# Kernel tuning notes

Measured on AMD Instinct MI355X. Metric: run time of the kernel, lower is better.

## Reference

```python
import jax, jax.numpy as jnp
import numpy as np

# ---- Cayley-Dickson octonion multiplication tables (SIGN_TABLE, WEIGHT_IDX) ----
def _cd_conj(a):
    n = a.shape[0]
    if n == 1:
        return a
    h = n // 2
    return np.concatenate([_cd_conj(a[:h]), -a[h:]])

def _cd_mul(a, b):
    n = a.shape[0]
    if n == 1:
        return a * b
    h = n // 2
    a1, a2 = a[:h], a[h:]
    c1, c2 = b[:h], b[h:]
    # (a1,a2)(c1,c2) = (a1 c1 - conj(c2) a2, c2 a1 + a2 conj(c1))
    return np.concatenate([_cd_mul(a1, c1) - _cd_mul(_cd_conj(c2), a2),
                           _cd_mul(c2, a1) + _cd_mul(a2, _cd_conj(c1))])

def _octonion_tables():
    signs = np.zeros((8, 8), dtype=np.float32)
    widx = np.zeros((8, 8), dtype=np.int32)
    for i in range(8):
        for j in range(8):
            ei = np.zeros(8); ei[i] = 1.0
            ej = np.zeros(8); ej[j] = 1.0
            p = _cd_mul(ei, ej)
            k = int(np.argmax(np.abs(p)))  # == i ^ j
            signs[i, j] = np.sign(p[k])
            widx[i, j] = k
    return jnp.asarray(signs), jnp.asarray(widx)

SIGNS, WIDX = _octonion_tables()


def ternary_ste(W):
    # BitNet-style per-matrix ternary quantization with straight-through estimator.
    s = jnp.mean(jnp.abs(W), axis=(-2, -1), keepdims=True) + 1e-8
    Wq = jnp.clip(jnp.round(W / s), -1.0, 1.0) * s
    return W + jax.lax.stop_gradient(Wq - W)


def oct_linear(x, W):
    # x: [B,T,C] split into 8 parts of C/8; out_i = sum_j sign[i,j] * x_j @ Wq[i^j]
    B, T, C = x.shape
    c8 = C // 8
    x8 = x.reshape(B, T, 8, c8)
    Wq = ternary_ste(W)          # [8, c8, c8]
    Wg = Wq[WIDX]                # [8, 8, c8, c8]
    out = jnp.einsum('ij,btjc,ijcd->btid', SIGNS, x8, Wg)
    return out.reshape(B, T, C)


def apply_rope(q, freqs_cos, freqs_sin):
    # q: [B,T,H,D]; complex pairs are (q[...,2k], q[...,2k+1])
    qe, qo = q[..., 0::2], q[..., 1::2]
    cos = freqs_cos[None, :, None, :]
    sin = freqs_sin[None, :, None, :]
    oe = qe * cos - qo * sin
    oo = qe * sin + qo * cos
    return jnp.stack([oe, oo], axis=-1).reshape(q.shape)


def setup_inputs() -> dict:
    key = jax.random.key(0)
    ks = jax.random.split(key, 8)
    B, T, C, H = 4, 1024, 2048, 16
    D = C // H           # 128
    c8 = C // 8          # 256
    x = jax.random.normal(ks[0], (B, T, C), dtype=jnp.float32)
    # RoPE tables (theta = 10000)
    inv = 1.0 / (10000.0 ** (jnp.arange(0, D, 2, dtype=jnp.float32) / D))
    ang = jnp.arange(T, dtype=jnp.float32)[:, None] * inv[None, :]   # [T, D/2]
    freqs_cos = jnp.cos(ang)
    freqs_sin = jnp.sin(ang)
    wq = jax.random.normal(ks[1], (8, c8, c8), dtype=jnp.float32) * 0.02
    wk = jax.random.normal(ks[2], (8, c8, c8), dtype=jnp.float32) * 0.02
    wv = jax.random.normal(ks[3], (8, c8, c8), dtype=jnp.float32) * 0.02
    wo = jax.random.normal(ks[4], (8, c8, c8), dtype=jnp.float32) * 0.02
    mixer_W = jax.random.normal(ks[5], (8, D, D), dtype=jnp.float32) * 0.02
    mixer_beta = jnp.ones((D,), dtype=jnp.float32) * 0.1
    return {"x": x, "freqs_cos": freqs_cos, "freqs_sin": freqs_sin,
            "wq": wq, "wk": wk, "wv": wv, "wo": wo,
            "mixer_W": mixer_W, "mixer_beta": mixer_beta}


def reference(x, freqs_cos, freqs_sin, wq, wk, wv, wo, mixer_W, mixer_beta):
    B, T, C = x.shape
    H = 16
    D = C // H
    q = oct_linear(x, wq).reshape(B, T, H, D)
    k = oct_linear(x, wk).reshape(B, T, H, D)
    v = oct_linear(x, wv).reshape(B, T, H, D)
    q = apply_rope(q, freqs_cos, freqs_sin)
    k = apply_rope(k, freqs_cos, freqs_sin)
    q, k, v = (jnp.transpose(t, (0, 2, 1, 3)) for t in (q, k, v))  # [B,H,T,D]
    # causal SDPA
    scale = 1.0 / jnp.sqrt(jnp.asarray(D, dtype=q.dtype))
    scores = jnp.einsum('bhqd,bhkd->bhqk', q, k) * scale
    mask = jnp.tril(jnp.ones((T, T), dtype=bool))
    scores = jnp.where(mask, scores, jnp.asarray(-1e30, dtype=scores.dtype))
    probs = jax.nn.softmax(scores, axis=-1)
    y = jnp.einsum('bhqk,bhkd->bhqd', probs, v)  # [B,H,T,D]
    # octonion head mixing per group of 8 heads
    G = H // 8
    y8 = y.reshape(B, G, 8, T, D)
    Wg = mixer_W[WIDX]  # [8,8,D,D]
    y8 = jnp.einsum('ij,bgjtd,ijde->bgite', SIGNS, y8, Wg) * mixer_beta
    y = y8.reshape(B, H, T, D)
    y = jnp.transpose(y, (0, 2, 1, 3)).reshape(B, T, C)
    return oct_linear(y, wo)
```

## Files before the change

### kernel.cpp

```cpp
#include <hip/hip_runtime.h>
#include <math.h>

#define CDIM 2048
#define QKVW 6144

typedef __bf16 bf16x8 __attribute__((ext_vector_type(8)));
typedef __bf16 bf16x4 __attribute__((ext_vector_type(4)));
typedef float  f32x4  __attribute__((ext_vector_type(4)));
typedef float  f32x16 __attribute__((ext_vector_type(16)));

__device__ __constant__ float SIGNS_c[64] = {
  1,  1,  1,  1,  1,  1,  1,  1,
  1, -1,  1, -1,  1, -1, -1,  1,
  1, -1, -1,  1,  1,  1, -1, -1,
  1,  1, -1, -1,  1, -1,  1, -1,
  1, -1, -1, -1, -1,  1,  1,  1,
  1,  1, -1,  1, -1, -1, -1,  1,
  1,  1,  1, -1, -1,  1, -1, -1,
  1, -1,  1,  1, -1, -1,  1, -1
};

__device__ __forceinline__ void load_lds16(const void* g, void* lp) {
  __builtin_amdgcn_global_load_lds(
      (const __attribute__((address_space(1))) unsigned int*)g,
      (__attribute__((address_space(3))) unsigned int*)lp, 16, 0, 0);
}

__device__ __forceinline__ void wg_barrier() {
  asm volatile("" ::: "memory");
  __builtin_amdgcn_s_barrier();
  asm volatile("" ::: "memory");
}

__device__ __forceinline__ unsigned pack2(float a, float b) {
  union { __bf16 h[2]; unsigned u; } x;
  x.h[0] = (__bf16)a; x.h[1] = (__bf16)b; return x.u;
}

__global__ __launch_bounds__(256)
void scale_part(const float* __restrict__ wq, const float* __restrict__ wk,
                const float* __restrict__ wv, const float* __restrict__ wo,
                double* __restrict__ part) {
  int bid = blockIdx.x;
  int which = bid >> 6, m = (bid >> 3) & 7, seg = bid & 7;
  const float* W = (which == 0) ? wq : (which == 1) ? wk : (which == 2) ? wv : wo;
  const float4* w4 = (const float4*)(W + (m << 16) + seg * 8192);
  double acc = 0.0;
  #pragma unroll
  for (int i = 0; i < 8; ++i) {
    float4 v = w4[threadIdx.x + i * 256];
    acc += (double)fabsf(v.x) + (double)fabsf(v.y) +
           (double)fabsf(v.z) + (double)fabsf(v.w);
  }
  __shared__ double red[256];
  red[threadIdx.x] = acc;
  __syncthreads();
  for (int s = 128; s > 0; s >>= 1) {
    if (threadIdx.x < s) red[threadIdx.x] += red[threadIdx.x + s];
    __syncthreads();
  }
  if (threadIdx.x == 0) part[bid] = red[0];
}

__global__ void scale_fin(const double* __restrict__ part, double* __restrict__ s8) {
  int t = threadIdx.x;
  if (t < 32) {
    double a = 0.0;
    #pragma unroll
    for (int i = 0; i < 8; ++i) a += part[t * 8 + i];
    s8[t] = a / 65536.0 + 1e-8;
  }
}

__global__ void build_oct3(const float* __restrict__ wq, const float* __restrict__ wk,
                           const float* __restrict__ wv, const double* __restrict__ s8,
                           __bf16* __restrict__ MT) {
  int z = blockIdx.y;
  const float* W = (z == 0) ? wq : (z == 1) ? wk : wv;
  const double* sp = s8 + z * 8;
  __bf16* out = MT + (size_t)z * 4194304;
  int idx = blockIdx.x * 256 + threadIdx.x;
  int row = idx & 2047, col = idx >> 11;
  int i = col >> 8, d = col & 255, j = row >> 8, c = row & 255;
  int m = i ^ j;
  double s = sp[m];
  double q = rint((double)W[(m << 16) + (c << 8) + d] / s);
  q = fmin(fmax(q, -1.0), 1.0);
  out[idx] = (__bf16)(SIGNS_c[i * 8 + j] * (float)(q * s));
}

__global__ void build_oct_T(const float* __restrict__ W, const double* __restrict__ s8,
                            __bf16* __restrict__ MT) {
  int idx = blockIdx.x * 256 + threadIdx.x;
  int row = idx & 2047, col = idx >> 11;
  int i = col >> 8, d = col & 255, j = row >> 8, c = row & 255;
  int m = i ^ j;
  double s = s8[m];
  double q = rint((double)W[(m << 16) + (c << 8) + d] / s);
  q = fmin(fmax(q, -1.0), 1.0);
  MT[idx] = (__bf16)(SIGNS_c[i * 8 + j] * (float)(q * s));
}

__global__ void build_mix_plain(const float* __restrict__ Wm, const float* __restrict__ beta,
                                __bf16* __restrict__ M) {
  int idx = blockIdx.x * 256 + threadIdx.x;
  int kl = idx & 1023, kpl = idx >> 10;
  int j = kpl >> 7, dd = kpl & 127;
  int i = kl >> 7, e = kl & 127;
  M[idx] = (__bf16)(SIGNS_c[i * 8 + j] * Wm[((i ^ j) << 14) + (dd << 7) + e] * beta[e]);
}

__global__ void cast_x(const float* __restrict__ x, __bf16* __restrict__ xb) {
  int i = blockIdx.x * 256 + threadIdx.x;
  float4 v = *(const float4*)(x + (size_t)i * 4);
  bf16x4 o;
  o[0] = (__bf16)v.x; o[1] = (__bf16)v.y; o[2] = (__bf16)v.z; o[3] = (__bf16)v.w;
  *(bf16x4*)(xb + (size_t)i * 4) = o;
}

__global__ __launch_bounds__(512, 2)
void gemm_qkv8(const __bf16* __restrict__ A, const __bf16* __restrict__ BT,
               __bf16* __restrict__ C) {
  __shared__ __align__(16) char smem[131072];
  int tid = threadIdx.x;
  int w = tid >> 6, l = tid & 63, hi = l >> 4, lo = l & 15;
  int wm = w >> 2, wn = w & 3;
  int lin = blockIdx.x;
  int xcd = lin & 7, idx = lin >> 3;
  int cy = xcd >> 2, cx = xcd & 3;
  int iby = idx >> 3, ibx = idx & 7;
  int bm = (cy * 8 + iby) * 256;
  int bn = (cx * 8 + ibx) * 192;
  const char* Ab = (const char*)A + (size_t)bm * 4096;
  const char* Bb = (const char*)BT + (size_t)bn * 4096;

  int sw = (((lo & 1) << 2) + hi) ^ (lo >> 1);

  int se_r[2], se_g[2], se_rb[2];
  #pragma unroll
  for (int q = 0; q < 2; ++q) {
    int e = q * 512 + tid;
    int lr = e >> 3, sl = e & 7;
    int x = sl ^ (lr & 7);
    se_r[q] = lr * 2 + (x >> 2);
    se_g[q] = x & 3;
    se_rb[q] = se_r[q] < 192 ? se_r[q] : 191;
  }
  int dstoff[2] = { (0 * 512 + w * 64) * 16, (1 * 512 + w * 64) * 16 };

  f32x4 acc[8][3];
  #pragma unroll
  for (int m = 0; m < 8; ++m)
    #pragma unroll
    for (int n = 0; n < 3; ++n) acc[m][n] = (f32x4){0.f, 0.f, 0.f, 0.f};
  bf16x8 bfr[3];

  #define STG(MAT, TT, KH) do {                                                  \
    char* dst_ = smem + ((TT) & 1) * 65536 + (MAT) * 32768 + (KH) * 16384;       \
    const char* gb_ = (MAT) ? Bb : Ab;                                           \
    _Pragma("unroll")                                                            \
    for (int q = 0; q < 2; ++q) {                                                \
      int r_ = (MAT) ? se_rb[q] : se_r[q];                                       \
      load_lds16(gb_ + (size_t)r_ * 4096 + ((TT) * 64 + (KH) * 32) * 2 + se_g[q] * 16, \
                 dst_ + dstoff[q]);                                              \
    }                                                                            \
  } while (0)

  #define QUAD(TT, KH, MSUB, READB) do {                                         \
    const char* ar_ = smem + ((TT) & 1) * 65536 + (KH) * 16384;                  \
    const char* br_ = ar_ + 32768;                                               \
    if (READB) {                                                                 \
      _Pragma("unroll")                                                          \
      for (int n = 0; n < 3; ++n)                                                \
        bfr[n] = *(const bf16x8*)(br_ + (wn * 24 + n * 8 + (lo >> 1)) * 128 + sw * 16); \
    }                                                                            \
    bf16x8 afr[4];                                                               \
    _Pragma("unroll")                                                            \
    for (int m = 0; m < 4; ++m)                                                  \
      afr[m] = *(const bf16x8*)(ar_ + (wm * 64 + (MSUB) * 32 + m * 8 + (lo >> 1)) * 128 + sw * 16); \
    __builtin_amdgcn_s_setprio(1);                                               \
    _Pragma("unroll")                                                            \
    for (int m = 0; m < 4; ++m)                                                  \
      _Pragma("unroll")                                                          \
      for (int n = 0; n < 3; ++n)                                                \
        acc[(MSUB) * 4 + m][n] =                                                 \
            __builtin_amdgcn_mfma_f32_16x16x32_bf16(afr[m], bfr[n], acc[(MSUB) * 4 + m][n], 0, 0, 0); \
    __builtin_amdgcn_s_setprio(0);                                               \
  } while (0)

  #define LGK0() asm volatile("s_waitcnt lgkmcnt(0)" ::: "memory")
  #define VMW8() asm volatile("s_waitcnt vmcnt(8)" ::: "memory")
  #define VMW4() asm volatile("s_waitcnt vmcnt(4)" ::: "memory")
  #define VMW0() asm volatile("s_waitcnt vmcnt(0)" ::: "memory")

  STG(0, 0, 0); STG(1, 0, 0);
  STG(0, 0, 1); STG(1, 0, 1);
  STG(0, 1, 0); STG(1, 1, 0);
  VMW8();
  wg_barrier();

  #define GITER(T0, LAST) do {                                                   \
     STG(0, (T0) + 1, 1); QUAD((T0), 0, 0, 1); wg_barrier();            \
     STG(1, (T0) + 1, 1); QUAD((T0), 0, 1, 0); LGK0(); VMW8(); wg_barrier(); \
     if (!(LAST)) { STG(0, (T0) + 2, 0); } QUAD((T0), 1, 0, 1); wg_barrier(); \
     if (!(LAST)) { STG(1, (T0) + 2, 0); } QUAD((T0), 1, 1, 0); LGK0(); \
              if (LAST) { VMW4(); } else { VMW8(); } wg_barrier();               \
     if (!(LAST)) { STG(0, (T0) + 2, 1); } QUAD((T0) + 1, 0, 0, 1); wg_barrier(); \
     if (!(LAST)) { STG(1, (T0) + 2, 1); } QUAD((T0) + 1, 0, 1, 0); LGK0(); \
              if (LAST) { VMW0(); } else { VMW8(); } wg_barrier();               \
     if (!(LAST)) { STG(0, (T0) + 3, 0); } QUAD((T0) + 1, 1, 0, 1); wg_barrier(); \
     if (!(LAST)) { STG(1, (T0) + 3, 0); } QUAD((T0) + 1, 1, 1, 0);     \
              if (!(LAST)) { LGK0(); VMW8(); wg_barrier(); }                     \
  } while (0)

  for (int i = 0; i < 15; ++i) GITER(2 * i, false);
  GITER(30, true);

  #undef GITER
  #undef STG
  #undef QUAD
  #undef VMW8
  #undef VMW4

  #pragma unroll
  for (int mm = 0; mm < 8; ++mm)
    #pragma unroll
    for (int n = 0; n < 3; ++n)
      #pragma unroll
      for (int r = 0; r < 4; ++r) {
        int row = bm + wm * 128 + mm * 16 + hi * 4 + r;
        int col = bn + wn * 48 + n * 16 + lo;
        C[(size_t)row * QKVW + col] = (__bf16)acc[mm][n][r];
      }
}

__global__ __launch_bounds__(512, 2)
void gemm_fin8(const __bf16* __restrict__ A, const __bf16* __restrict__ BT,
               float* __restrict__ C) {
  __shared__ __align__(16) char smem[98304];
  int tid = threadIdx.x;
  int w = tid >> 6, l = tid & 63, hi = l >> 4, lo = l & 15;
  int wm = w >> 2, wn = w & 3;
  int lin = blockIdx.x;
  int xcd = lin & 7, idx = lin >> 3;
  int cy = xcd >> 1, cx = xcd & 1;
  int iby = idx >> 2, ibx = idx & 3;
  int bm = (cy * 8 + iby) * 128;
  int bn = (cx * 4 + ibx) * 256;
  const char* Ab = (const char*)A + (size_t)bm * 12288;
  const char* Bb = (const char*)BT + (size_t)bn * 4096;

  int sw = (((lo & 1) << 2) + hi) ^ (lo >> 1);

  int se_r[2], se_g[2];
  #pragma unroll
  for (int q = 0; q < 2; ++q) {
    int e = q * 512 + tid;
    int lr = e >> 3, sl = e & 7;
    int x = sl ^ (lr & 7);
    se_r[q] = lr * 2 + (x >> 2);
    se_g[q] = x & 3;
  }
  int dstoff[2] = { (0 * 512 + w * 64) * 16, (1 * 512 + w * 64) * 16 };

  f32x4 acc[4][4];
  #pragma unroll
  for (int m = 0; m < 4; ++m)
    #pragma unroll
    for (int n = 0; n < 4; ++n) acc[m][n] = (f32x4){0.f, 0.f, 0.f, 0.f};
  bf16x8 bfr[4];

  #define STG(MAT, TT, KH) do {                                                  \
    char* ab_ = smem + ((TT) & 1) * 49152;                                       \
    char* dst_ = (MAT) ? (ab_ + 16384 + (KH) * 16384) : (ab_ + (KH) * 8192);     \
    const char* gb_ = (MAT) ? Bb : Ab;                                           \
    size_t ld_ = (MAT) ? 4096 : 12288;                                           \
    int nq_ = (MAT) ? 2 : 1;                                                     \
    _Pragma("unroll")                                                            \
    for (int q = 0; q < 2; ++q)                                                  \
      if (q < nq_)                                                               \
        load_lds16(gb_ + (size_t)se_r[q] * ld_ + ((TT) * 64 + (KH) * 32) * 2 + se_g[q] * 16, \
                   dst_ + dstoff[q]);                                            \
  } while (0)

  #define QUAD(TT, KH, MSUB, READB) do {                                         \
    const char* ab_ = smem + ((TT) & 1) * 49152;                                 \
    const char* ar_ = ab_ + (KH) * 8192;                                         \
    const char* br_ = ab_ + 16384 + (KH) * 16384;                                \
    if (READB) {                                                                 \
      _Pragma("unroll")                                                          \
      for (int n = 0; n < 4; ++n)                                                \
        bfr[n] = *(const bf16x8*)(br_ + (wn * 32 + n * 8 + (lo >> 1)) * 128 + sw * 16); \
    }                                                                            \
    bf16x8 afr[2];                                                               \
    _Pragma("unroll")                                                            \
    for (int m = 0; m < 2; ++m)                                                  \
      afr[m] = *(const bf16x8*)(ar_ + (wm * 32 + (MSUB) * 16 + m * 8 + (lo >> 1)) * 128 + sw * 16); \
    __builtin_amdgcn_s_setprio(1);                                               \
    _Pragma("unroll")                                                            \
    for (int m = 0; m < 2; ++m)                                                  \
      _Pragma("unroll")                                                          \
      for (int n = 0; n < 4; ++n)                                                \
        acc[(MSUB) * 2 + m][n] =                                                 \
            __builtin_amdgcn_mfma_f32_16x16x32_bf16(afr[m], bfr[n], acc[(MSUB) * 2 + m][n], 0, 0, 0); \
    __builtin_amdgcn_s_setprio(0);                                               \
  } while (0)

  #define VMW6() asm volatile("s_waitcnt vmcnt(6)" ::: "memory")
  #define VMW3() asm volatile("s_waitcnt vmcnt(3)" ::: "memory")

  STG(0, 0, 0); STG(1, 0, 0);
  STG(0, 0, 1); STG(1, 0, 1);
  STG(0, 1, 0); STG(1, 1, 0);
  VMW6();
  wg_barrier();

  #define GITER(T0, LAST) do {                                                   \
     STG(0, (T0) + 1, 1); QUAD((T0), 0, 0, 1); wg_barrier();            \
     STG(1, (T0) + 1, 1); QUAD((T0), 0, 1, 0); LGK0(); VMW6(); wg_barrier(); \
     if (!(LAST)) { STG(0, (T0) + 2, 0); } QUAD((T0), 1, 0, 1); wg_barrier(); \
     if (!(LAST)) { STG(1, (T0) + 2, 0); } QUAD((T0), 1, 1, 0); LGK0(); \
              if (LAST) { VMW3(); } else { VMW6(); } wg_barrier();               \
     if (!(LAST)) { STG(0, (T0) + 2, 1); } QUAD((T0) + 1, 0, 0, 1); wg_barrier(); \
     if (!(LAST)) { STG(1, (T0) + 2, 1); } QUAD((T0) + 1, 0, 1, 0); LGK0(); \
              if (LAST) { VMW0(); } else { VMW6(); } wg_barrier();               \
     if (!(LAST)) { STG(0, (T0) + 3, 0); } QUAD((T0) + 1, 1, 0, 1); wg_barrier(); \
     if (!(LAST)) { STG(1, (T0) + 3, 0); } QUAD((T0) + 1, 1, 1, 0);     \
              if (!(LAST)) { LGK0(); VMW6(); wg_barrier(); }                     \
  } while (0)

  for (int i = 0; i < 15; ++i) GITER(2 * i, false);
  GITER(30, true);

  #undef GITER
  #undef STG
  #undef QUAD
  #undef VMW6
  #undef VMW3
  #undef LGK0
  #undef VMW0

  #pragma unroll
  for (int mm = 0; mm < 4; ++mm)
    #pragma unroll
    for (int n = 0; n < 4; ++n)
      #pragma unroll
      for (int r = 0; r < 4; ++r) {
        int row = bm + wm * 64 + mm * 16 + hi * 4 + r;
        int col = bn + wn * 64 + n * 16 + lo;
        C[(size_t)row * 2048 + col] = acc[mm][n][r];
      }
}

template<int BN, int NBY, int NBX, int CBY, int CBX, int KLEN, int LDA, int OUT_BF16>
__global__ __launch_bounds__(512, 2)
void gemm_ps(const __bf16* __restrict__ A, const __bf16* __restrict__ BT,
             void* __restrict__ Cout, int az, int cz, int ldc) {
  constexpr int FN = BN / 64;
  constexpr int LB = (BN > 128) ? 2 : 1;
  constexpr int VC = 2 + LB;
  constexpr int BUFSZ = 16384 + 8192 * LB;
  constexpr int CGX = NBX / CBX;
  static_assert((NBY / CBY) * CGX == 8, "chunk grid must be 8 XCDs");
  __shared__ __align__(16) char smem[2 * BUFSZ];
  int tid = threadIdx.x;
  int w = tid >> 6, l = tid & 63, hi = l >> 4, lo = l & 15;
  int wm = w >> 2, wn = w & 3;
  int lin = blockIdx.x;
  int xcd = lin & 7, idx = lin >> 3;
  int cy = xcd / CGX, cx = xcd % CGX;
  int iby = idx / CBX, ibx = idx % CBX;
  int bm = (cy * CBY + iby) * 256;
  int bn = (cx * CBX + ibx) * BN;
  const char* Ab = (const char*)(A + (size_t)blockIdx.y * az) + (size_t)bm * LDA * 2;
  const char* Bb = (const char*)BT + (size_t)bn * KLEN * 2;

  int sw = (((lo & 1) << 2) + hi) ^ (lo >> 1);
  int base_a = (wm * 64 + (lo >> 1)) * 128 + sw * 16;
  int base_b = 16384 + (wn * (BN / 8) + (lo >> 1)) * 128 + sw * 16;

  int se_r[2], se_g[2];
  #pragma unroll
  for (int q = 0; q < 2; ++q) {
    int e = q * 512 + tid;
    int lr = e >> 3, sl = e & 7;
    int x = sl ^ (lr & 7);
    se_r[q] = lr * 2 + (x >> 2);
    se_g[q] = x & 3;
  }
  int dstoff[2] = { (0 * 512 + w * 64) * 16, (1 * 512 + w * 64) * 16 };

  f32x4 acc[8][FN];
  #pragma unroll
  for (int m = 0; m < 8; ++m)
    #pragma unroll
    for (int n = 0; n < FN; ++n) acc[m][n] = (f32x4){0.f, 0.f, 0.f, 0.f};

  #define STAGE(BUFI, K0) do {                                                   \
    char* As_ = smem + (BUFI) * BUFSZ;                                           \
    char* Bs_ = As_ + 16384;                                                     \
    _Pragma("unroll")                                                            \
    for (int q = 0; q < 2; ++q)                                                  \
      load_lds16(Ab + (size_t)se_r[q] * (LDA * 2) + (size_t)(K0) * 2 + se_g[q] * 16, \
                 As_ + dstoff[q]);                                               \
    _Pragma("unroll")                                                            \
    for (int q = 0; q < LB; ++q)                                                 \
      load_lds16(Bb + (size_t)se_r[q] * (KLEN * 2) + (size_t)(K0) * 2 + se_g[q] * 16, \
                 Bs_ + dstoff[q]);                                               \
  } while (0)

  #define WAITVC() do {                                                \
    if constexpr (VC == 4) asm volatile("s_waitcnt vmcnt(4)" ::: "memory"); \
    else                   asm volatile("s_waitcnt vmcnt(3)" ::: "memory"); \
  } while (0)

  constexpr int NT = KLEN / 32;
  STAGE(0, 0);
  STAGE(1, 32);
  WAITVC();
  wg_barrier();

  for (int t = 0; t < NT; ++t) {
    char* buf = smem + (t & 1) * BUFSZ;
    bf16x8 bfr[FN], afr[8];
    #pragma unroll
    for (int n = 0; n < FN; ++n) bfr[n] = *(const bf16x8*)(buf + base_b + n * 1024);
    #pragma unroll
    for (int m = 0; m < 8; ++m) afr[m] = *(const bf16x8*)(buf + base_a + m * 1024);
    __builtin_amdgcn_s_setprio(1);
    #pragma unroll
    for (int m = 0; m < 4; ++m)
      #pragma unroll
      for (int n = 0; n < FN; ++n)
        acc[m][n] = __builtin_amdgcn_mfma_f32_16x16x32_bf16(afr[m], bfr[n], acc[m][n], 0, 0, 0);
    __builtin_amdgcn_s_setprio(0);
    asm volatile("s_waitcnt lgkmcnt(0)" ::: "memory");
    wg_barrier();

    if (t + 2 < NT) STAGE(t & 1, (t + 2) * 32);
    __builtin_amdgcn_s_setprio(1);
    #pragma unroll
    for (int m = 4; m < 8; ++m)
      #pragma unroll
      for (int n = 0; n < FN; ++n)
        acc[m][n] = __builtin_amdgcn_mfma_f32_16x16x32_bf16(afr[m], bfr[n], acc[m][n], 0, 0, 0);
    __builtin_amdgcn_s_setprio(0);
    if (t + 2 < NT) { WAITVC(); }
    else            { asm volatile("s_waitcnt vmcnt(0)" ::: "memory"); }
    wg_barrier();
  }
  #undef STAGE
  #undef WAITVC

  #pragma unroll
  for (int m = 0; m < 8; ++m)
    #pragma unroll
    for (int n = 0; n < FN; ++n)
      #pragma unroll
      for (int r = 0; r < 4; ++r) {
        int row = bm + wm * 64 + m * 16 + hi * 4 + r;
        int col = bn + wn * (BN / 4) + n * 16 + lo;
        if (OUT_BF16)
          ((__bf16*)Cout)[(size_t)blockIdx.y * cz + (size_t)(bm + wm * 128 + m * 16 + hi * 4 + r) * ldc + col] = (__bf16)acc[m][n][r];
        else
          ((float*)Cout)[(size_t)blockIdx.y * cz + (size_t)(bm + wm * 128 + m * 16 + hi * 4 + r) * ldc + col] = acc[m][n][r];
      }
}

__global__ void rope_bf16(__bf16* __restrict__ QKV,
                          const float* __restrict__ fc, const float* __restrict__ fs) {
  int idx = blockIdx.x * 256 + threadIdx.x;
  int pg = idx & 15;
  int h = (idx >> 4) & 15;
  int n = idx >> 8;
  int t = n & 1023;
  float4 c4 = *(const float4*)(fc + t * 64 + pg * 4);
  float4 s4 = *(const float4*)(fs + t * 64 + pg * 4);
  float c[4] = {c4.x, c4.y, c4.z, c4.w};
  float s[4] = {s4.x, s4.y, s4.z, s4.w};
  size_t ofs = (size_t)n * QKVW + h * 128 + pg * 8;
  bf16x8 q = *(bf16x8*)(QKV + ofs);
  bf16x8 k = *(bf16x8*)(QKV + 2048 + ofs);
  bf16x8 oq, ok;
  #pragma unroll
  for (int j = 0; j < 4; ++j) {
    float x = (float)q[2 * j], y = (float)q[2 * j + 1];
    oq[2 * j]     = (__bf16)(x * c[j] - y * s[j]);
    oq[2 * j + 1] = (__bf16)(x * s[j] + y * c[j]);
    float u = (float)k[2 * j], vv = (float)k[2 * j + 1];
    ok[2 * j]     = (__bf16)(u * c[j] - vv * s[j]);
    ok[2 * j + 1] = (__bf16)(u * s[j] + vv * c[j]);
  }
  *(bf16x8*)(QKV + ofs) = oq;
  *(bf16x8*)(QKV + 2048 + ofs) = ok;
}

__global__ __launch_bounds__(256)
void transpose_v(const __bf16* __restrict__ QKV, __bf16* __restrict__ VT) {
  __shared__ __bf16 tile[64][136];
  int tid = threadIdx.x;
  int tt = blockIdx.x;
  int bh = blockIdx.y;
  int b = bh >> 4, h = bh & 15;
  int t0 = tt * 64;
  #pragma unroll
  for (int q = 0; q < 4; ++q) {
    int i = q * 256 + tid;
    int tr = i >> 4, u = i & 15;
    bf16x8 v = *(const bf16x8*)(QKV + (size_t)(b * 1024 + t0 + tr) * QKVW + 4096 + h * 128 + u * 8);
    *(bf16x8*)&tile[tr][u * 8] = v;
  }
  __syncthreads();
  #pragma unroll
  for (int q = 0; q < 4; ++q) {
    int i = q * 256 + tid;
    int d = i >> 3, tu = i & 7;
    bf16x8 o;
    #pragma unroll
    for (int jj = 0; jj < 8; ++jj) o[jj] = tile[tu * 8 + jj][d];
    *(bf16x8*)(VT + ((size_t)bh * 128 + d) * 1024 + t0 + tu * 8) = o;
  }
}

__global__ __launch_bounds__(256, 2)
void attn_mfma2(__bf16* __restrict__ QKV, const __bf16* __restrict__ VT) {
  __shared__ __align__(16) char smem[65536];
  int tid = threadIdx.x;
  int w = tid >> 6, l = tid & 63;
  int lo = l & 31, hv = l >> 5;
  int wgid = blockIdx.x;
  int xcd = wgid & 7, idx = wgid >> 3;
  int s = idx & 7, j = s >> 1, odd = s & 1, hi5 = idx >> 5;
  int base = hi5 ? 7 - j : j;
  int qt = odd ? 7 - base : base;
  int bh = xcd * 8 + (idx >> 3);
  int b = bh >> 4, h = bh & 15;
  int qb = qt * 128;
  int wq0 = qb + w * 32;
  int qrow = wq0 + lo;
  const __bf16* qp = QKV + (size_t)(b * 1024 + qrow) * QKVW + h * 128;
  bf16x8 qf[8];
  #pragma unroll
  for (int c = 0; c < 8; ++c) qf[c] = *(const bf16x8*)(qp + c * 16 + hv * 8);

  f32x16 o[4];
  #pragma unroll
  for (int n = 0; n < 4; ++n)
    #pragma unroll
    for (int r = 0; r < 16; ++r) o[n][r] = 0.f;
  float mrun = -1e30f, lrun = 0.f;
  const float SCL = 0.08838834764831845f * 1.4426950408889634f;
  int src0 = lo, src1 = 32 + lo;
  int nt = 2 * qt + 2;

  #define ASTAGE(BUF, KT) do {                                                   \
    _Pragma("unroll")                                                            \
    for (int i = 0; i < 4; ++i) {                                                \
      int e = i * 256 + tid;                                                     \
      int row = e >> 4, g = e & 15;                                              \
      int gs = g ^ (row & 7);                                                    \
      const char* src = (const char*)QKV +                                       \
          ((size_t)(b * 1024 + (KT) * 64 + row) * QKVW + 2048 + h * 128) * 2 + gs * 16; \
      load_lds16(src, smem + (BUF) * 16384 + (i * 256 + w * 64) * 16);           \
    }                                                                            \
    _Pragma("unroll")                                                            \
    for (int i = 0; i < 4; ++i) {                                                \
      int e = i * 256 + tid;                                                     \
      int row = e >> 3, g = e & 7;                                               \
      int gs = g ^ (row & 7);                                                    \
      const char* src = (const char*)VT +                                        \
          ((size_t)(bh * 128 + row) * 1024 + (KT) * 64) * 2 + gs * 16;           \
      load_lds16(src, smem + 32768 + (BUF) * 16384 + (i * 256 + w * 64) * 16);   \
    }                                                                            \
  } while (0)

  ASTAGE(0, 0);
  asm volatile("s_waitcnt vmcnt(0)" ::: "memory");
  wg_barrier();

  for (int kt = 0; kt < nt; ++kt) {
    int cur = kt & 1;
    if (kt + 1 < nt) ASTAGE(cur ^ 1, kt + 1);
    int k0 = kt * 64;
    char* Ks  = smem + cur * 16384;
    char* VTs = smem + 32768 + cur * 16384;

    if (k0 <= wq0 + 31) {
      f32x16 sT[2];
      #pragma unroll
      for (int kk = 0; kk < 2; ++kk) {
        #pragma unroll
        for (int r = 0; r < 16; ++r) sT[kk][r] = 0.f;
        #pragma unroll
        for (int c = 0; c < 8; ++c) {
          bf16x8 kf = *(const bf16x8*)(Ks + (kk * 32 + lo) * 256 + (((2 * c + hv) ^ (lo & 7)) * 16));
          sT[kk] = __builtin_amdgcn_mfma_f32_32x32x16_bf16(kf, qf[c], sT[kk], 0, 0, 0);
        }
      }
      bool diag = (k0 + 63 > wq0);
      float pv[2][16];
      #pragma unroll
      for (int kk = 0; kk < 2; ++kk)
        #pragma unroll
        for (int r = 0; r < 16; ++r) {
          float v = sT[kk][r] * SCL;
          if (diag) {
            int kg = k0 + kk * 32 + (r & 3) + 8 * (r >> 2) + 4 * hv;
            if (kg > qrow) v = -1e30f;
          }
          pv[kk][r] = v;
        }
      float mx = pv[0][0];
      #pragma unroll
      for (int kk = 0; kk < 2; ++kk)
        #pragma unroll
        for (int r = 0; r < 16; ++r) mx = fmaxf(mx, pv[kk][r]);
      mx = fmaxf(mx, __shfl_xor(mx, 32, 64));
      if (!__all(mx <= mrun + 8.f)) {
        float mnew = fmaxf(mrun, mx);
        float fac = exp2f(mrun - mnew);
        lrun *= fac;
        #pragma unroll
        for (int n = 0; n < 4; ++n)
          #pragma unroll
          for (int r = 0; r < 16; ++r) o[n][r] *= fac;
        mrun = mnew;
      }
      float rs = 0.f;
      #pragma unroll
      for (int kk = 0; kk < 2; ++kk)
        #pragma unroll
        for (int r = 0; r < 16; ++r) {
          float p = exp2f(pv[kk][r] - mrun);
          pv[kk][r] = p;
          rs += p;
        }
      rs += __shfl_xor(rs, 32, 64);
      lrun += rs;

      unsigned pk[2][4][2];
      #pragma unroll
      for (int kk = 0; kk < 2; ++kk)
        #pragma unroll
        for (int m = 0; m < 4; ++m)
          #pragma unroll
          for (int u = 0; u < 2; ++u)
            pk[kk][m][u] = pack2(pv[kk][m * 4 + 2 * u], pv[kk][m * 4 + 2 * u + 1]);

      #pragma unroll
      for (int kk = 0; kk < 2; ++kk) {
        #pragma unroll
        for (int s2 = 0; s2 < 2; ++s2) {
          unsigned a0 = __shfl(pk[kk][2 * s2][0], src0, 64);
          unsigned b0 = __shfl(pk[kk][2 * s2 + 1][0], src0, 64);
          unsigned a1 = __shfl(pk[kk][2 * s2][1], src0, 64);
          unsigned b1 = __shfl(pk[kk][2 * s2 + 1][1], src0, 64);
          unsigned a2 = __shfl(pk[kk][2 * s2][0], src1, 64);
          unsigned b2 = __shfl(pk[kk][2 * s2 + 1][0], src1, 64);
          unsigned a3 = __shfl(pk[kk][2 * s2][1], src1, 64);
          unsigned b3 = __shfl(pk[kk][2 * s2 + 1][1], src1, 64);
          union { unsigned u[4]; bf16x8 v; } pb;
          pb.u[0] = hv ? b0 : a0;
          pb.u[1] = hv ? b1 : a1;
          pb.u[2] = hv ? b2 : a2;
          pb.u[3] = hv ? b3 : a3;
          int ks16 = 2 * kk + s2;
          #pragma unroll
          for (int n = 0; n < 4; ++n) {
            bf16x8 vf = *(const bf16x8*)(VTs + (n * 32 + lo) * 128 +
                                         (((2 * ks16 + hv) ^ (lo & 7)) * 16));
            o[n] = __builtin_amdgcn_mfma_f32_32x32x16_bf16(vf, pb.v, o[n], 0, 0, 0);
          }
        }
      }
    }
    asm volatile("s_waitcnt vmcnt(0)" ::: "memory");
    wg_barrier();
  }
  #undef ASTAGE

  float inv = 1.f / lrun;
  __bf16* op = QKV + (size_t)(b * 1024 + qrow) * QKVW + h * 128;
  #pragma unroll
  for (int n = 0; n < 4; ++n)
    #pragma unroll
    for (int m4 = 0; m4 < 4; ++m4) {
      bf16x4 ov;
      #pragma unroll
      for (int jj = 0; jj < 4; ++jj) ov[jj] = (__bf16)(o[n][m4 * 4 + jj] * inv);
      *(bf16x4*)(op + n * 32 + 8 * m4 + 4 * hv) = ov;
    }
}

extern "C" void kernel_launch(void* const* d_in, const int* in_sizes, int n_in,
                              void* d_out, int out_size, void* d_ws, size_t ws_size,
                              hipStream_t stream) {
  const float* x    = (const float*)d_in[0];
  const float* fc   = (const float*)d_in[1];
  const float* fs   = (const float*)d_in[2];
  const float* wq   = (const float*)d_in[3];
  const float* wk   = (const float*)d_in[4];
  const float* wv   = (const float*)d_in[5];
  const float* wo   = (const float*)d_in[6];
  const float* wm   = (const float*)d_in[7];
  const float* beta = (const float*)d_in[8];

  char* wsb = (char*)d_ws;
  __bf16* xb      = (__bf16*)(wsb);
  __bf16* MTqkv   = (__bf16*)(wsb + 16777216L);
  __bf16* QKV     = (__bf16*)(wsb + 41943040L);
  __bf16* VTb     = (__bf16*)(wsb + 92274688L);
  double* s8      = (double*)(wsb + 109051904L);
  double* part    = (double*)(wsb + 109052160L);
  __bf16* MTwo    = (__bf16*)(wsb);
  __bf16* BTfused = (__bf16*)(wsb + 8388608L);
  __bf16* MTmixP  = MTqkv;

  dim3 blk(256);

  cast_x<<<8192, blk, 0, stream>>>(x, xb);
  scale_part<<<256, blk, 0, stream>>>(wq, wk, wv, wo, part);
  scale_fin<<<1, dim3(64), 0, stream>>>(part, s8);
  build_oct3<<<dim3(16384, 3), blk, 0, stream>>>(wq, wk, wv, s8, MTqkv);

  gemm_qkv8<<<512, dim3(512), 0, stream>>>(xb, MTqkv, QKV);

  build_oct_T<<<16384, blk, 0, stream>>>(wo, s8 + 24, MTwo);
  build_mix_plain<<<4096, blk, 0, stream>>>(wm, beta, MTmixP);
  gemm_ps<128, 8, 8, 2, 4, 1024, 2048, 1>
      <<<dim3(64, 2), dim3(512), 0, stream>>>(MTwo, MTmixP, BTfused, 1024, 1024, 2048);

  rope_bf16<<<4096, blk, 0, stream>>>(QKV, fc, fs);
  transpose_v<<<dim3(16, 64), blk, 0, stream>>>(QKV, VTb);

  attn_mfma2<<<dim3(512), blk, 0, stream>>>(QKV, VTb);

  gemm_fin8<<<256, dim3(512), 0, stream>>>(QKV, BTfused, (float*)d_out);
}
```

Before: 305.9 us.

## Fuse RoPE into QKV GEMM epilogue, merge cast with scale reduction

Applies rotary embedding inside the QKV GEMM epilogue, using a lane shuffle to fetch the pair partner, so the standalone rope kernel and its extra read and write of Q/K are gone. The x cast and the weight-scale partial reduction are merged into one launch, and the scale finish kernel also writes reciprocals so the build kernels multiply instead of doing a double divide. The multiply by a reciprocal can round differently from the divide at ternary rounding boundaries. RoPE is now computed in fp32 before the bf16 store, which differs slightly from the old order of storing bf16 first and then rotating.

Result: slower. 321.0 us (+5.0%).

```diff
diff --git a/kernel.cpp b/kernel.cpp
--- a/kernel.cpp
+++ b/kernel.cpp
@@ -38,10 +38,20 @@
 }
 
 __global__ __launch_bounds__(256)
-void scale_part(const float* __restrict__ wq, const float* __restrict__ wk,
+void cast_scale(const float* __restrict__ x, __bf16* __restrict__ xb,
+                const float* __restrict__ wq, const float* __restrict__ wk,
                 const float* __restrict__ wv, const float* __restrict__ wo,
                 double* __restrict__ part) {
-  int bid = blockIdx.x;
+  __shared__ double red[256];
+  if (blockIdx.x < 8192) {
+    int i = blockIdx.x * 256 + threadIdx.x;
+    float4 v = *(const float4*)(x + (size_t)i * 4);
+    bf16x4 o;
+    o[0] = (__bf16)v.x; o[1] = (__bf16)v.y; o[2] = (__bf16)v.z; o[3] = (__bf16)v.w;
+    *(bf16x4*)(xb + (size_t)i * 4) = o;
+    return;
+  }
+  int bid = blockIdx.x - 8192;
   int which = bid >> 6, m = (bid >> 3) & 7, seg = bid & 7;
   const float* W = (which == 0) ? wq : (which == 1) ? wk : (which == 2) ? wv : wo;
   const float4* w4 = (const float4*)(W + (m << 16) + seg * 8192);
@@ -52,7 +62,6 @@
     acc += (double)fabsf(v.x) + (double)fabsf(v.y) +
            (double)fabsf(v.z) + (double)fabsf(v.w);
   }
-  __shared__ double red[256];
   red[threadIdx.x] = acc;
   __syncthreads();
   for (int s = 128; s > 0; s >>= 1) {
@@ -62,43 +71,45 @@
   if (threadIdx.x == 0) part[bid] = red[0];
 }
 
-__global__ void scale_fin(const double* __restrict__ part, double* __restrict__ s8) {
+__global__ void scale_fin(const double* __restrict__ part, double* __restrict__ s8,
+                          double* __restrict__ rs8) {
   int t = threadIdx.x;
   if (t < 32) {
     double a = 0.0;
     #pragma unroll
     for (int i = 0; i < 8; ++i) a += part[t * 8 + i];
-    s8[t] = a / 65536.0 + 1e-8;
+    double s = a / 65536.0 + 1e-8;
+    s8[t] = s;
+    rs8[t] = 1.0 / s;
   }
 }
 
 __global__ void build_oct3(const float* __restrict__ wq, const float* __restrict__ wk,
                            const float* __restrict__ wv, const double* __restrict__ s8,
-                           __bf16* __restrict__ MT) {
+                           const double* __restrict__ rs8, __bf16* __restrict__ MT) {
   int z = blockIdx.y;
   const float* W = (z == 0) ? wq : (z == 1) ? wk : wv;
   const double* sp = s8 + z * 8;
+  const double* rp = rs8 + z * 8;
   __bf16* out = MT + (size_t)z * 4194304;
   int idx = blockIdx.x * 256 + threadIdx.x;
   int row = idx & 2047, col = idx >> 11;
   int i = col >> 8, d = col & 255, j = row >> 8, c = row & 255;
   int m = i ^ j;
-  double s = sp[m];
-  double q = rint((double)W[(m << 16) + (c << 8) + d] / s);
+  double q = rint((double)W[(m << 16) + (c << 8) + d] * rp[m]);
   q = fmin(fmax(q, -1.0), 1.0);
-  out[idx] = (__bf16)(SIGNS_c[i * 8 + j] * (float)(q * s));
+  out[idx] = (__bf16)(SIGNS_c[i * 8 + j] * (float)(q * sp[m]));
 }
 
 __global__ void build_oct_T(const float* __restrict__ W, const double* __restrict__ s8,
-                            __bf16* __restrict__ MT) {
+                            const double* __restrict__ rs8, __bf16* __restrict__ MT) {
   int idx = blockIdx.x * 256 + threadIdx.x;
   int row = idx & 2047, col = idx >> 11;
   int i = col >> 8, d = col & 255, j = row >> 8, c = row & 255;
   int m = i ^ j;
-  double s = s8[m];
-  double q = rint((double)W[(m << 16) + (c << 8) + d] / s);
+  double q = rint((double)W[(m << 16) + (c << 8) + d] * rs8[m]);
   q = fmin(fmax(q, -1.0), 1.0);
-  MT[idx] = (__bf16)(SIGNS_c[i * 8 + j] * (float)(q * s));
+  MT[idx] = (__bf16)(SIGNS_c[i * 8 + j] * (float)(q * s8[m]));
 }
 
 __global__ void build_mix_plain(const float* __restrict__ Wm, const float* __restrict__ beta,
@@ -110,16 +121,9 @@
   M[idx] = (__bf16)(SIGNS_c[i * 8 + j] * Wm[((i ^ j) << 14) + (dd << 7) + e] * beta[e]);
 }
 
-__global__ void cast_x(const float* __restrict__ x, __bf16* __restrict__ xb) {
-  int i = blockIdx.x * 256 + threadIdx.x;
-  float4 v = *(const float4*)(x + (size_t)i * 4);
-  bf16x4 o;
-  o[0] = (__bf16)v.x; o[1] = (__bf16)v.y; o[2] = (__bf16)v.z; o[3] = (__bf16)v.w;
-  *(bf16x4*)(xb + (size_t)i * 4) = o;
-}
-
 __global__ __launch_bounds__(512, 2)
 void gemm_qkv8(const __bf16* __restrict__ A, const __bf16* __restrict__ BT,
+               const float* __restrict__ fc, const float* __restrict__ fs,
                __bf16* __restrict__ C) {
   __shared__ __align__(16) char smem[131072];
   int tid = threadIdx.x;
@@ -221,17 +225,31 @@
   #undef QUAD
   #undef VMW8
   #undef VMW4
+  #undef LGK0
+  #undef VMW0
 
   #pragma unroll
   for (int mm = 0; mm < 8; ++mm)
     #pragma unroll
-    for (int n = 0; n < 3; ++n)
+    for (int n = 0; n < 3; ++n) {
+      int col = bn + wn * 48 + n * 16 + lo;
+      int isqk = (col < 4096);
+      int p = (col & 127) >> 1;
+      int evenl = ((col & 1) == 0);
       #pragma unroll
       for (int r = 0; r < 4; ++r) {
         int row = bm + wm * 128 + mm * 16 + hi * 4 + r;
-        int col = bn + wn * 48 + n * 16 + lo;
-        C[(size_t)row * QKVW + col] = (__bf16)acc[mm][n][r];
+        float v = acc[mm][n][r];
+        float other = __shfl_xor(v, 1, 64);
+        if (isqk) {
+          int t = row & 1023;
+          float c = fc[t * 64 + p];
+          float s = fs[t * 64 + p];
+          v = evenl ? (v * c - other * s) : (other * s + v * c);
+        }
+        C[(size_t)row * QKVW + col] = (__bf16)v;
       }
+    }
 }
 
 __global__ __launch_bounds__(512, 2)
@@ -306,8 +324,10 @@
     __builtin_amdgcn_s_setprio(0);                                               \
   } while (0)
 
+  #define LGK0() asm volatile("s_waitcnt lgkmcnt(0)" ::: "memory")
   #define VMW6() asm volatile("s_waitcnt vmcnt(6)" ::: "memory")
   #define VMW3() asm volatile("s_waitcnt vmcnt(3)" ::: "memory")
+  #define VMW0() asm volatile("s_waitcnt vmcnt(0)" ::: "memory")
 
   STG(0, 0, 0); STG(1, 0, 0);
   STG(0, 0, 1); STG(1, 0, 1);
@@ -458,41 +478,13 @@
     for (int n = 0; n < FN; ++n)
       #pragma unroll
       for (int r = 0; r < 4; ++r) {
-        int row = bm + wm * 64 + m * 16 + hi * 4 + r;
+        int row = bm + wm * 128 + m * 16 + hi * 4 + r;
         int col = bn + wn * (BN / 4) + n * 16 + lo;
         if (OUT_BF16)
-          ((__bf16*)Cout)[(size_t)blockIdx.y * cz + (size_t)(bm + wm * 128 + m * 16 + hi * 4 + r) * ldc + col] = (__bf16)acc[m][n][r];
+          ((__bf16*)Cout)[(size_t)blockIdx.y * cz + (size_t)row * ldc + col] = (__bf16)acc[m][n][r];
         else
-          ((float*)Cout)[(size_t)blockIdx.y * cz + (size_t)(bm + wm * 128 + m * 16 + hi * 4 + r) * ldc + col] = acc[m][n][r];
+          ((float*)Cout)[(size_t)blockIdx.y * cz + (size_t)row * ldc + col] = acc[m][n][r];
       }
-}
-
-__global__ void rope_bf16(__bf16* __restrict__ QKV,
-                          const float* __restrict__ fc, const float* __restrict__ fs) {
-  int idx = blockIdx.x * 256 + threadIdx.x;
-  int pg = idx & 15;
-  int h = (idx >> 4) & 15;
-  int n = idx >> 8;
-  int t = n & 1023;
-  float4 c4 = *(const float4*)(fc + t * 64 + pg * 4);
-  float4 s4 = *(const float4*)(fs + t * 64 + pg * 4);
-  float c[4] = {c4.x, c4.y, c4.z, c4.w};
-  float s[4] = {s4.x, s4.y, s4.z, s4.w};
-  size_t ofs = (size_t)n * QKVW + h * 128 + pg * 8;
-  bf16x8 q = *(bf16x8*)(QKV + ofs);
-  bf16x8 k = *(bf16x8*)(QKV + 2048 + ofs);
-  bf16x8 oq, ok;
-  #pragma unroll
-  for (int j = 0; j < 4; ++j) {
-    float x = (float)q[2 * j], y = (float)q[2 * j + 1];
-    oq[2 * j]     = (__bf16)(x * c[j] - y * s[j]);
-    oq[2 * j + 1] = (__bf16)(x * s[j] + y * c[j]);
-    float u = (float)k[2 * j], vv = (float)k[2 * j + 1];
-    ok[2 * j]     = (__bf16)(u * c[j] - vv * s[j]);
-    ok[2 * j + 1] = (__bf16)(u * s[j] + vv * c[j]);
-  }
-  *(bf16x8*)(QKV + ofs) = oq;
-  *(bf16x8*)(QKV + 2048 + ofs) = ok;
 }
 
 __global__ __launch_bounds__(256)
@@ -712,25 +704,24 @@
   __bf16* VTb     = (__bf16*)(wsb + 92274688L);
   double* s8      = (double*)(wsb + 109051904L);
   double* part    = (double*)(wsb + 109052160L);
+  double* rs8     = (double*)(wsb + 109054208L);
   __bf16* MTwo    = (__bf16*)(wsb);
   __bf16* BTfused = (__bf16*)(wsb + 8388608L);
   __bf16* MTmixP  = MTqkv;
 
   dim3 blk(256);
 
-  cast_x<<<8192, blk, 0, stream>>>(x, xb);
-  scale_part<<<256, blk, 0, stream>>>(wq, wk, wv, wo, part);
-  scale_fin<<<1, dim3(64), 0, stream>>>(part, s8);
-  build_oct3<<<dim3(16384, 3), blk, 0, stream>>>(wq, wk, wv, s8, MTqkv);
-
-  gemm_qkv8<<<512, dim3(512), 0, stream>>>(xb, MTqkv, QKV);
-
-  build_oct_T<<<16384, blk, 0, stream>>>(wo, s8 + 24, MTwo);
+  cast_scale<<<8448, blk, 0, stream>>>(x, xb, wq, wk, wv, wo, part);
+  scale_fin<<<1, dim3(64), 0, stream>>>(part, s8, rs8);
+  build_oct3<<<dim3(16384, 3), blk, 0, stream>>>(wq, wk, wv, s8, rs8, MTqkv);
+
+  gemm_qkv8<<<512, dim3(512), 0, stream>>>(xb, MTqkv, fc, fs, QKV);
+
+  build_oct_T<<<16384, blk, 0, stream>>>(wo, s8 + 24, rs8 + 24, MTwo);
   build_mix_plain<<<4096, blk, 0, stream>>>(wm, beta, MTmixP);
   gemm_ps<128, 8, 8, 2, 4, 1024, 2048, 1>
       <<<dim3(64, 2), dim3(512), 0, stream>>>(MTwo, MTmixP, BTfused, 1024, 1024, 2048);
 
-  rope_bf16<<<4096, blk, 0, stream>>>(QKV, fc, fs);
   transpose_v<<<dim3(16, 64), blk, 0, stream>>>(QKV, VTb);
 
   attn_mfma2<<<dim3(512), blk, 0, stream>>>(QKV, VTb);
```
